# Optimization experiments

Measured on AMD Instinct MI355X. Metric: run time of the kernel, lower is better.

## Reference

```python
import jax, jax.numpy as jnp
import numpy as np

IN_F = 512
OUT_F = 512
ALPHA = 0.2  # LeakyReLU negative slope
# dropout p=0.1 is a no-op at inference (training=False), so omitted


def setup_inputs() -> dict:
    key = jax.random.key(0)
    k1, k2, k3 = jax.random.split(key, 3)
    B, N = 16, 1024
    x = jax.random.normal(k1, (B, N, IN_F), dtype=jnp.float32)
    # xavier_uniform with gain=1.414
    limW = 1.414 * np.sqrt(6.0 / (IN_F + OUT_F))
    W = jax.random.uniform(k2, (IN_F, OUT_F), minval=-limW, maxval=limW, dtype=jnp.float32)
    lima = 1.414 * np.sqrt(6.0 / (2 * OUT_F + 1))
    a = jax.random.uniform(k3, (2 * OUT_F, 1), minval=-lima, maxval=lima, dtype=jnp.float32)
    beta = jnp.ones((1,), dtype=jnp.float32)
    return {"x": x, "W": W, "a": a, "beta": beta}


def reference(x, W, a, beta):
    # h: [B, N, F]
    h = jnp.matmul(x, W)
    # Split attention vector: e_ij = leakyrelu(h_i . a1 + h_j . a2)
    a1 = a[:OUT_F, 0]   # [F]
    a2 = a[OUT_F:, 0]   # [F]
    s1 = jnp.einsum('bnf,f->bn', h, a1)  # [B, N]
    s2 = jnp.einsum('bnf,f->bn', h, a2)  # [B, N]
    e = s1[:, :, None] + s2[:, None, :]  # [B, N, N]
    e = jnp.where(e > 0, e, ALPHA * e)   # LeakyReLU
    attention = jax.nn.softmax(e, axis=2)
    h_prime = jnp.einsum('bnm,bmf->bnf', attention, h)
    out = jax.nn.elu(h_prime + beta * h)
    return out
```

## Files before the change

### kernel.cpp

```cpp
#include <hip/hip_runtime.h>

using u16 = unsigned short;
using u32 = unsigned int;

#define ALPHA 0.2f
#define LOG2E 1.4426950408889634f

typedef __bf16 bf16x8 __attribute__((ext_vector_type(8)));
typedef float f32x4 __attribute__((ext_vector_type(4)));
typedef float f32x16 __attribute__((ext_vector_type(16)));

__device__ __forceinline__ u16 f2bf(float f) {
  u32 u = __builtin_bit_cast(u32, f);
  u += 0x7FFFu + ((u >> 16) & 1u);
  return (u16)(u >> 16);
}
__device__ __forceinline__ float bf2f(u16 h) {
  u32 u = ((u32)h) << 16;
  return __builtin_bit_cast(float, u);
}
__device__ __forceinline__ void gload_lds16(const void* g, void* l) {
  __builtin_amdgcn_global_load_lds((__attribute__((address_space(1))) void*)g,
                                   (__attribute__((address_space(3))) void*)l,
                                   16, 0, 0);
}

__global__ __launch_bounds__(256) void k_cast_wT(const float* __restrict__ W, u16* __restrict__ wbt) {
  int idx = blockIdx.x * 256 + threadIdx.x;
  int k = idx >> 9, n = idx & 511;
  wbt[n * 512 + k] = f2bf(W[idx]);
}

__global__ __launch_bounds__(256, 2) void k_gemm1(const float* __restrict__ x, const u16* __restrict__ wbt,
                                                  const float* __restrict__ a,
                                                  u16* __restrict__ hbf, u16* __restrict__ hbt,
                                                  float* __restrict__ s1p, float* __restrict__ s2p) {
  __shared__ __attribute__((aligned(16))) char lds[73728];
  __shared__ __attribute__((aligned(16))) float a_l[256];

  const int t = threadIdx.x;
  const int lane = t & 63;
  const int w = t >> 6;
  const int l31 = lane & 31, lhi = lane >> 5;
  const int rb = w >> 1, cg = w & 1;
  const int tile_m = blockIdx.x >> 2;
  const int cb = blockIdx.x & 3;
  const int row0 = tile_m * 128;
  const int col0 = cb * 128;

  a_l[t] = (t < 128) ? a[col0 + t] : a[512 + col0 + (t - 128)];

  f32x16 acc[2][2];
#pragma unroll
  for (int i = 0; i < 2; ++i)
#pragma unroll
    for (int j = 0; j < 2; ++j)
#pragma unroll
      for (int r = 0; r < 16; ++r) acc[i][j][r] = 0.f;

#define STAGE_G1(kt, Ab, Bb)                                                              \
  {                                                                                       \
    const int k0_ = (kt) * 32;                                                            \
    _Pragma("unroll")                                                                     \
    for (int i = 0; i < 4; ++i) {                                                         \
      int G = i * 256 + t;                                                                \
      int row = G >> 3, ks = G & 7;                                                       \
      gload_lds16(x + (size_t)(row0 + row) * 512 + k0_ + ((ks ^ (row & 7)) * 4),          \
                  (Ab) + (size_t)(i * 256 + w * 64) * 16);                                \
    }                                                                                     \
    _Pragma("unroll")                                                                     \
    for (int i = 0; i < 2; ++i) {                                                         \
      int G = i * 256 + t;                                                                \
      int col = G >> 2, ks = G & 3;                                                       \
      gload_lds16(wbt + (size_t)(col0 + col) * 512 + k0_ + ((ks ^ ((col >> 1) & 3)) * 8), \
                  (Bb) + (size_t)(i * 256 + w * 64) * 16);                                \
    }                                                                                     \
  }

#define COMPUTE_G1(Ab, Bb)                                                                         \
  {                                                                                                \
    _Pragma("unroll")                                                                              \
    for (int ks = 0; ks < 2; ++ks) {                                                               \
      bf16x8 af[2];                                                                                \
      _Pragma("unroll")                                                                            \
      for (int sub = 0; sub < 2; ++sub) {                                                          \
        const int arow = rb * 64 + sub * 32 + l31;                                                 \
        const int kg = ks * 4 + lhi * 2;                                                           \
        f32x4 fa0 = *reinterpret_cast<const f32x4*>((Ab) + (size_t)(arow * 8 + (kg ^ (arow & 7))) * 16); \
        f32x4 fa1 = *reinterpret_cast<const f32x4*>((Ab) + (size_t)(arow * 8 + ((kg + 1) ^ (arow & 7))) * 16); \
        _Pragma("unroll")                                                                          \
        for (int j = 0; j < 4; ++j) {                                                              \
          af[sub][j] = (__bf16)fa0[j];                                                             \
          af[sub][j + 4] = (__bf16)fa1[j];                                                         \
        }                                                                                          \
      }                                                                                            \
      bf16x8 bfr[2];                                                                               \
      _Pragma("unroll")                                                                            \
      for (int bt = 0; bt < 2; ++bt) {                                                             \
        const int bcol = cg * 64 + bt * 32 + l31;                                                  \
        const int kslot = (ks * 2 + lhi) ^ ((bcol >> 1) & 3);                                      \
        bfr[bt] = *reinterpret_cast<const bf16x8*>((Bb) + (size_t)(bcol * 4 + kslot) * 16);        \
      }                                                                                            \
      _Pragma("unroll")                                                                            \
      for (int sub = 0; sub < 2; ++sub)                                                            \
        _Pragma("unroll")                                                                          \
        for (int bt = 0; bt < 2; ++bt)                                                             \
          acc[sub][bt] = __builtin_amdgcn_mfma_f32_32x32x16_bf16(af[sub], bfr[bt], acc[sub][bt], 0, 0, 0); \
    }                                                                                              \
  }

  char* Ac = lds;             char* Bc = lds + 49152;
  char* An = lds + 16384;     char* Bn = lds + 57344;
  char* As = lds + 32768;     char* Bs = lds + 65536;

  STAGE_G1(0, Ac, Bc);
  STAGE_G1(1, An, Bn);
  __builtin_amdgcn_sched_barrier(0);
  asm volatile("s_waitcnt vmcnt(6) lgkmcnt(0)" ::: "memory");
  __builtin_amdgcn_s_barrier();
  __builtin_amdgcn_sched_barrier(0);

#pragma unroll 1
  for (int kt = 0; kt < 14; ++kt) {
    STAGE_G1(kt + 2, As, Bs);
    COMPUTE_G1(Ac, Bc);
    __builtin_amdgcn_sched_barrier(0);
    asm volatile("s_waitcnt vmcnt(6)" ::: "memory");
    __builtin_amdgcn_s_barrier();
    __builtin_amdgcn_sched_barrier(0);
    char* ta = Ac; Ac = An; An = As; As = ta;
    char* tb = Bc; Bc = Bn; Bn = Bs; Bs = tb;
  }
  COMPUTE_G1(Ac, Bc);
  __builtin_amdgcn_sched_barrier(0);
  asm volatile("s_waitcnt vmcnt(0)" ::: "memory");
  __builtin_amdgcn_s_barrier();
  __builtin_amdgcn_sched_barrier(0);
  COMPUTE_G1(An, Bn);
#undef STAGE_G1
#undef COMPUTE_G1

  __syncthreads();

  u16* lT = (u16*)lds;
#pragma unroll
  for (int sub = 0; sub < 2; ++sub)
#pragma unroll
    for (int bt = 0; bt < 2; ++bt) {
      const int col = cg * 64 + bt * 32 + l31;
#pragma unroll
      for (int r = 0; r < 16; ++r) {
        int row = rb * 64 + sub * 32 + (r & 3) + 8 * (r >> 2) + 4 * lhi;
        lT[row * 136 + col] = f2bf(acc[sub][bt][r]);
      }
    }
  __syncthreads();

#pragma unroll
  for (int i = 0; i < 8; ++i) {
    int G = i * 256 + t;
    int row = G >> 4, g = G & 15;
    uint4 v = *reinterpret_cast<const uint4*>(&lT[row * 136 + g * 8]);
    *reinterpret_cast<uint4*>(&hbf[(size_t)(row0 + row) * 512 + col0 + g * 8]) = v;
  }
  const int bb = row0 >> 10;
  const int nb = row0 & 1023;
#pragma unroll
  for (int i = 0; i < 8; ++i) {
    int G = i * 256 + t;
    int col = G & 127, rg = G >> 7;
    u32 wd[4];
#pragma unroll
    for (int jj = 0; jj < 4; ++jj) {
      u16 lo = lT[(rg * 8 + 2 * jj) * 136 + col];
      u16 hi = lT[(rg * 8 + 2 * jj + 1) * 136 + col];
      wd[jj] = (u32)lo | ((u32)hi << 16);
    }
    uint4 o = {wd[0], wd[1], wd[2], wd[3]};
    *reinterpret_cast<uint4*>(&hbt[(size_t)(bb * 512 + col0 + col) * 1024 + nb + rg * 8]) = o;
  }
  {
    const int r2 = t >> 1, half = t & 1;
    float d1 = 0.f, d2 = 0.f;
#pragma unroll
    for (int i = 0; i < 8; ++i) {
      uint4 v = *reinterpret_cast<const uint4*>(&lT[r2 * 136 + half * 64 + i * 8]);
      u32 wds[4] = {v.x, v.y, v.z, v.w};
#pragma unroll
      for (int j = 0; j < 8; ++j) {
        float h = bf2f((u16)(wds[j >> 1] >> ((j & 1) * 16)));
        d1 += h * a_l[half * 64 + i * 8 + j];
        d2 += h * a_l[128 + half * 64 + i * 8 + j];
      }
    }
    d1 += __shfl_xor(d1, 1);
    d2 += __shfl_xor(d2, 1);
    if (half == 0) {
      s1p[cb * 16384 + row0 + r2] = d1;
      s2p[cb * 16384 + row0 + r2] = d2;
    }
  }
}

__global__ __launch_bounds__(256) void k_reduce(const float* __restrict__ s1p, const float* __restrict__ s2p,
                                                float* __restrict__ s1L, float* __restrict__ s2L) {
  int id = blockIdx.x * 256 + threadIdx.x;
  float d1 = s1p[id] + s1p[16384 + id] + s1p[32768 + id] + s1p[49152 + id];
  float d2 = s2p[id] + s2p[16384 + id] + s2p[32768 + id] + s2p[49152 + id];
  s1L[id] = d1 * LOG2E;
  s2L[id] = d2 * LOG2E;
}

__global__ __launch_bounds__(256) void k_denom(const float* __restrict__ s1Lg, const float* __restrict__ s2Lg,
                                               float* __restrict__ invg) {
  const int lane = threadIdx.x & 63;
  const int w = threadIdx.x >> 6;
  const int row = blockIdx.x * 4 + w;
  const int b = row >> 10;
  const float s1v = s1Lg[row];
  const float* s2p = s2Lg + ((size_t)b << 10);
  float sum = 0.f;
#pragma unroll
  for (int i = 0; i < 16; ++i) {
    float e = s1v + s2p[i * 64 + lane];
    sum += exp2f(fmaxf(e, ALPHA * e));
  }
#pragma unroll
  for (int off = 32; off > 0; off >>= 1) sum += __shfl_xor(sum, off);
  if (lane == 0) invg[row] = 1.0f / sum;
}

__global__ __launch_bounds__(256, 2) void k_attn(const u16* __restrict__ hbt, const u16* __restrict__ hbf,
                                                 const float* __restrict__ s1Lg, const float* __restrict__ s2Lg,
                                                 const float* __restrict__ invg, const float* __restrict__ betag,
                                                 float* __restrict__ out) {
  __shared__ __attribute__((aligned(16))) u16 bbuf[3][8192];
  __shared__ __attribute__((aligned(16))) float e1_l[1024];
  __shared__ __attribute__((aligned(16))) float e2_l[1024];
  const int t = threadIdx.x;
  const int lane = t & 63;
  const int w = t >> 6;
  const int l31 = lane & 31, lhi = lane >> 5;

  const int B = blockIdx.x;
  const int b = (B & 7) * 2 + ((B >> 3) & 1);
  const int j = B >> 4;
  const int n0 = (j >> 2) * 128;
  const int c0 = (j & 3) * 128;

  const u16* hb = hbt + (size_t)b * 512 * 1024;

  for (int i = t; i < 1024; i += 256) {
    float v = s2Lg[b * 1024 + i];
    e1_l[i] = exp2f(v);
    e2_l[i] = exp2f(ALPHA * v);
  }
  const int myrow = n0 + w * 32 + l31;
  const float s1v = s1Lg[b * 1024 + myrow];
  const float c1 = exp2f(s1v), c2 = exp2f(ALPHA * s1v);

#define STAGE_ATTN(mt, dst)                                                        \
  {                                                                                \
    _Pragma("unroll")                                                              \
    for (int i = 0; i < 4; ++i) {                                                  \
      int G = i * 256 + t;                                                         \
      int c = G >> 3, g = G & 7;                                                   \
      gload_lds16(hb + (size_t)(c0 + c) * 1024 + (mt) * 64 + ((g ^ (c & 7)) * 8),  \
                  (char*)(dst) + (size_t)(i * 256 + w * 64) * 16);                 \
    }                                                                              \
  }

#define COMPUTE_ATTN(mt, src)                                                                 \
  {                                                                                           \
    _Pragma("unroll")                                                                         \
    for (int step = 0; step < 4; ++step) {                                                    \
      const int mo = (mt) * 64 + step * 16 + lhi * 8;                                         \
      f32x4 ea = *reinterpret_cast<const f32x4*>(&e1_l[mo]);                                  \
      f32x4 eb = *reinterpret_cast<const f32x4*>(&e1_l[mo + 4]);                              \
      f32x4 fa = *reinterpret_cast<const f32x4*>(&e2_l[mo]);                                  \
      f32x4 fb = *reinterpret_cast<const f32x4*>(&e2_l[mo + 4]);                              \
      bf16x8 af;                                                                              \
      _Pragma("unroll")                                                                       \
      for (int q = 0; q < 4; ++q) {                                                           \
        af[q] = (__bf16)fmaxf(c1 * ea[q], c2 * fa[q]);                                        \
        af[q + 4] = (__bf16)fmaxf(c1 * eb[q], c2 * fb[q]);                                    \
      }                                                                                       \
      const int gm = step * 2 + lhi;                                                          \
      _Pragma("unroll")                                                                       \
      for (int ct = 0; ct < 4; ++ct) {                                                        \
        const int c = ct * 32 + l31;                                                          \
        bf16x8 bv = *reinterpret_cast<const bf16x8*>(&(src)[c * 64 + ((gm ^ (c & 7)) * 8)]);  \
        acc[ct] = __builtin_amdgcn_mfma_f32_32x32x16_bf16(af, bv, acc[ct], 0, 0, 0);          \
      }                                                                                       \
    }                                                                                         \
  }

  f32x16 acc[4];
#pragma unroll
  for (int ct = 0; ct < 4; ++ct)
#pragma unroll
    for (int r = 0; r < 16; ++r) acc[ct][r] = 0.f;

  u16* bcur = bbuf[0];
  u16* bnxt = bbuf[1];
  u16* bstg = bbuf[2];

  STAGE_ATTN(0, bcur);
  STAGE_ATTN(1, bnxt);
  __builtin_amdgcn_sched_barrier(0);
  asm volatile("s_waitcnt vmcnt(4) lgkmcnt(0)" ::: "memory");
  __builtin_amdgcn_s_barrier();
  __builtin_amdgcn_sched_barrier(0);

#pragma unroll 1
  for (int mt = 0; mt < 14; ++mt) {
    STAGE_ATTN(mt + 2, bstg);
    COMPUTE_ATTN(mt, bcur);
    __builtin_amdgcn_sched_barrier(0);
    asm volatile("s_waitcnt vmcnt(4)" ::: "memory");
    __builtin_amdgcn_s_barrier();
    __builtin_amdgcn_sched_barrier(0);
    u16* tmp = bcur; bcur = bnxt; bnxt = bstg; bstg = tmp;
  }
  COMPUTE_ATTN(14, bcur);
  __builtin_amdgcn_sched_barrier(0);
  asm volatile("s_waitcnt vmcnt(0)" ::: "memory");
  __builtin_amdgcn_s_barrier();
  __builtin_amdgcn_sched_barrier(0);
  COMPUTE_ATTN(15, bnxt);
#undef STAGE_ATTN
#undef COMPUTE_ATTN

  const float beta = betag[0];
  const float* invb = invg + b * 1024;
  const u16* hf = hbf + (size_t)b * 1024 * 512;
#pragma unroll
  for (int ct = 0; ct < 4; ++ct) {
    const int colv = c0 + ct * 32 + l31;
#pragma unroll
    for (int rg = 0; rg < 4; ++rg) {
      const int rowb = n0 + w * 32 + rg * 8 + lhi * 4;
      f32x4 iv = *reinterpret_cast<const f32x4*>(&invb[rowb]);
#pragma unroll
      for (int q = 0; q < 4; ++q) {
        float hv = bf2f(hf[(size_t)(rowb + q) * 512 + colv]);
        float xv = acc[ct][rg * 4 + q] * iv[q] + beta * hv;
        out[((size_t)b * 1024 + rowb + q) * 512 + colv] = xv > 0.f ? xv : __expf(xv) - 1.0f;
      }
    }
  }
}

extern "C" void kernel_launch(void* const* d_in, const int* in_sizes, int n_in,
                              void* d_out, int out_size, void* d_ws, size_t ws_size,
                              hipStream_t stream) {
  const float* x = (const float*)d_in[0];
  const float* W = (const float*)d_in[1];
  const float* a = (const float*)d_in[2];
  const float* beta = (const float*)d_in[3];
  float* out = (float*)d_out;

  char* ws = (char*)d_ws;
  u16* hbf = (u16*)ws;
  u16* hbt = (u16*)(ws + (16u << 20));
  u16* wbt = (u16*)(ws + (32u << 20));
  float* s1p = (float*)(ws + (32u << 20) + (512u << 10));
  float* s2p = (float*)(ws + (32u << 20) + (768u << 10));
  float* s1L = (float*)(ws + (33u << 20));
  float* s2L = (float*)(ws + (33u << 20) + (64u << 10));
  float* inv = (float*)(ws + (33u << 20) + (128u << 10));

  k_cast_wT<<<1024, 256, 0, stream>>>(W, wbt);
  k_gemm1<<<512, 256, 0, stream>>>(x, wbt, a, hbf, hbt, s1p, s2p);
  k_reduce<<<64, 256, 0, stream>>>(s1p, s2p, s1L, s2L);
  k_denom<<<4096, 256, 0, stream>>>(s1L, s2L, inv);
  k_attn<<<512, 256, 0, stream>>>(hbt, hbf, s1L, s2L, inv, beta, out);
}
```

Measured before the change: 74.59 us.

## Fuse softmax denominator into attention kernel and pre-swizzle H into MFMA fragment layout

Removes the separate k_denom kernel by summing the unnormalised attention weights in registers inside k_attn and reducing them per row. gemm1 now writes the transposed H in a fragment-ready tiled layout, so k_attn loads B operands straight from global memory into registers with one-step prefetch, replacing the LDS triple-buffered staging and its barriers. It also remaps gemm1 block indices so neighbouring blocks share column tiles. This drops a kernel launch and LDS traffic, but leaves the global loads with less latency hiding. The row sums now come from bf16-bound fp32 values rather than the separate exact pass.

```diff
diff --git a/kernel.cpp b/kernel.cpp
--- a/kernel.cpp
+++ b/kernel.cpp
@@ -31,9 +31,10 @@
   wbt[n * 512 + k] = f2bf(W[idx]);
 }
 
+
 __global__ __launch_bounds__(256, 2) void k_gemm1(const float* __restrict__ x, const u16* __restrict__ wbt,
                                                   const float* __restrict__ a,
-                                                  u16* __restrict__ hbf, u16* __restrict__ hbt,
+                                                  u16* __restrict__ hbf, u16* __restrict__ hbt2,
                                                   float* __restrict__ s1p, float* __restrict__ s2p) {
   __shared__ __attribute__((aligned(16))) char lds[73728];
   __shared__ __attribute__((aligned(16))) float a_l[256];
@@ -43,8 +44,9 @@
   const int w = t >> 6;
   const int l31 = lane & 31, lhi = lane >> 5;
   const int rb = w >> 1, cg = w & 1;
-  const int tile_m = blockIdx.x >> 2;
-  const int cb = blockIdx.x & 3;
+  const int g = blockIdx.x;
+  const int cb = (g >> 3) & 3;
+  const int tile_m = (g & 7) | ((g >> 5) << 3);
   const int row0 = tile_m * 128;
   const int col0 = cb * 128;
 
@@ -89,9 +91,9 @@
         f32x4 fa0 = *reinterpret_cast<const f32x4*>((Ab) + (size_t)(arow * 8 + (kg ^ (arow & 7))) * 16); \
         f32x4 fa1 = *reinterpret_cast<const f32x4*>((Ab) + (size_t)(arow * 8 + ((kg + 1) ^ (arow & 7))) * 16); \
         _Pragma("unroll")                                                                          \
-        for (int j = 0; j < 4; ++j) {                                                              \
-          af[sub][j] = (__bf16)fa0[j];                                                             \
-          af[sub][j + 4] = (__bf16)fa1[j];                                                         \
+        for (int jj = 0; jj < 4; ++jj) {                                                           \
+          af[sub][jj] = (__bf16)fa0[jj];                                                           \
+          af[sub][jj + 4] = (__bf16)fa1[jj];                                                       \
         }                                                                                          \
       }                                                                                            \
       bf16x8 bfr[2];                                                                               \
@@ -159,12 +161,13 @@
 #pragma unroll
   for (int i = 0; i < 8; ++i) {
     int G = i * 256 + t;
-    int row = G >> 4, g = G & 15;
-    uint4 v = *reinterpret_cast<const uint4*>(&lT[row * 136 + g * 8]);
-    *reinterpret_cast<uint4*>(&hbf[(size_t)(row0 + row) * 512 + col0 + g * 8]) = v;
+    int row = G >> 4, gg = G & 15;
+    uint4 v = *reinterpret_cast<const uint4*>(&lT[row * 136 + gg * 8]);
+    *reinterpret_cast<uint4*>(&hbf[(size_t)(row0 + row) * 512 + col0 + gg * 8]) = v;
   }
   const int bb = row0 >> 10;
   const int nb = row0 & 1023;
+  u16* hb2 = hbt2 + (size_t)bb * 524288;
 #pragma unroll
   for (int i = 0; i < 8; ++i) {
     int G = i * 256 + t;
@@ -177,7 +180,10 @@
       wd[jj] = (u32)lo | ((u32)hi << 16);
     }
     uint4 o = {wd[0], wd[1], wd[2], wd[3]};
-    *reinterpret_cast<uint4*>(&hbt[(size_t)(bb * 512 + col0 + col) * 1024 + nb + rg * 8]) = o;
+    const int m0 = nb + rg * 8;
+    const int f = col0 + col;
+    size_t idx = (size_t)(m0 >> 4) * 8192 + (size_t)(f >> 5) * 512 + (size_t)((m0 >> 3) & 1) * 256 + (size_t)(f & 31) * 8;
+    *reinterpret_cast<uint4*>(&hb2[idx]) = o;
   }
   {
     const int r2 = t >> 1, half = t & 1;
@@ -187,10 +193,10 @@
       uint4 v = *reinterpret_cast<const uint4*>(&lT[r2 * 136 + half * 64 + i * 8]);
       u32 wds[4] = {v.x, v.y, v.z, v.w};
 #pragma unroll
-      for (int j = 0; j < 8; ++j) {
-        float h = bf2f((u16)(wds[j >> 1] >> ((j & 1) * 16)));
-        d1 += h * a_l[half * 64 + i * 8 + j];
-        d2 += h * a_l[128 + half * 64 + i * 8 + j];
+      for (int jj = 0; jj < 8; ++jj) {
+        float h = bf2f((u16)(wds[jj >> 1] >> ((jj & 1) * 16)));
+        d1 += h * a_l[half * 64 + i * 8 + jj];
+        d2 += h * a_l[128 + half * 64 + i * 8 + jj];
       }
     }
     d1 += __shfl_xor(d1, 1);
@@ -211,32 +217,12 @@
   s2L[id] = d2 * LOG2E;
 }
 
-__global__ __launch_bounds__(256) void k_denom(const float* __restrict__ s1Lg, const float* __restrict__ s2Lg,
-                                               float* __restrict__ invg) {
-  const int lane = threadIdx.x & 63;
-  const int w = threadIdx.x >> 6;
-  const int row = blockIdx.x * 4 + w;
-  const int b = row >> 10;
-  const float s1v = s1Lg[row];
-  const float* s2p = s2Lg + ((size_t)b << 10);
-  float sum = 0.f;
-#pragma unroll
-  for (int i = 0; i < 16; ++i) {
-    float e = s1v + s2p[i * 64 + lane];
-    sum += exp2f(fmaxf(e, ALPHA * e));
-  }
-#pragma unroll
-  for (int off = 32; off > 0; off >>= 1) sum += __shfl_xor(sum, off);
-  if (lane == 0) invg[row] = 1.0f / sum;
-}
-
-__global__ __launch_bounds__(256, 2) void k_attn(const u16* __restrict__ hbt, const u16* __restrict__ hbf,
+__global__ __launch_bounds__(256, 2) void k_attn(const u16* __restrict__ hbt2, const u16* __restrict__ hbf,
                                                  const float* __restrict__ s1Lg, const float* __restrict__ s2Lg,
-                                                 const float* __restrict__ invg, const float* __restrict__ betag,
-                                                 float* __restrict__ out) {
-  __shared__ __attribute__((aligned(16))) u16 bbuf[3][8192];
+                                                 const float* __restrict__ betag, float* __restrict__ out) {
   __shared__ __attribute__((aligned(16))) float e1_l[1024];
   __shared__ __attribute__((aligned(16))) float e2_l[1024];
+  __shared__ __attribute__((aligned(16))) float inv_l[128];
   const int t = threadIdx.x;
   const int lane = t & 63;
   const int w = t >> 6;
@@ -248,99 +234,81 @@
   const int n0 = (j >> 2) * 128;
   const int c0 = (j & 3) * 128;
 
-  const u16* hb = hbt + (size_t)b * 512 * 1024;
+  const u16* hb2 = hbt2 + (size_t)b * 524288;
 
   for (int i = t; i < 1024; i += 256) {
     float v = s2Lg[b * 1024 + i];
     e1_l[i] = exp2f(v);
     e2_l[i] = exp2f(ALPHA * v);
   }
+
   const int myrow = n0 + w * 32 + l31;
   const float s1v = s1Lg[b * 1024 + myrow];
   const float c1 = exp2f(s1v), c2 = exp2f(ALPHA * s1v);
 
-#define STAGE_ATTN(mt, dst)                                                        \
-  {                                                                                \
-    _Pragma("unroll")                                                              \
-    for (int i = 0; i < 4; ++i) {                                                  \
-      int G = i * 256 + t;                                                         \
-      int c = G >> 3, g = G & 7;                                                   \
-      gload_lds16(hb + (size_t)(c0 + c) * 1024 + (mt) * 64 + ((g ^ (c & 7)) * 8),  \
-                  (char*)(dst) + (size_t)(i * 256 + w * 64) * 16);                 \
-    }                                                                              \
-  }
-
-#define COMPUTE_ATTN(mt, src)                                                                 \
-  {                                                                                           \
-    _Pragma("unroll")                                                                         \
-    for (int step = 0; step < 4; ++step) {                                                    \
-      const int mo = (mt) * 64 + step * 16 + lhi * 8;                                         \
-      f32x4 ea = *reinterpret_cast<const f32x4*>(&e1_l[mo]);                                  \
-      f32x4 eb = *reinterpret_cast<const f32x4*>(&e1_l[mo + 4]);                              \
-      f32x4 fa = *reinterpret_cast<const f32x4*>(&e2_l[mo]);                                  \
-      f32x4 fb = *reinterpret_cast<const f32x4*>(&e2_l[mo + 4]);                              \
-      bf16x8 af;                                                                              \
-      _Pragma("unroll")                                                                       \
-      for (int q = 0; q < 4; ++q) {                                                           \
-        af[q] = (__bf16)fmaxf(c1 * ea[q], c2 * fa[q]);                                        \
-        af[q + 4] = (__bf16)fmaxf(c1 * eb[q], c2 * fb[q]);                                    \
-      }                                                                                       \
-      const int gm = step * 2 + lhi;                                                          \
-      _Pragma("unroll")                                                                       \
-      for (int ct = 0; ct < 4; ++ct) {                                                        \
-        const int c = ct * 32 + l31;                                                          \
-        bf16x8 bv = *reinterpret_cast<const bf16x8*>(&(src)[c * 64 + ((gm ^ (c & 7)) * 8)]);  \
-        acc[ct] = __builtin_amdgcn_mfma_f32_32x32x16_bf16(af, bv, acc[ct], 0, 0, 0);          \
-      }                                                                                       \
-    }                                                                                         \
-  }
-
   f32x16 acc[4];
 #pragma unroll
   for (int ct = 0; ct < 4; ++ct)
 #pragma unroll
     for (int r = 0; r < 16; ++r) acc[ct][r] = 0.f;
-
-  u16* bcur = bbuf[0];
-  u16* bnxt = bbuf[1];
-  u16* bstg = bbuf[2];
-
-  STAGE_ATTN(0, bcur);
-  STAGE_ATTN(1, bnxt);
-  __builtin_amdgcn_sched_barrier(0);
-  asm volatile("s_waitcnt vmcnt(4) lgkmcnt(0)" ::: "memory");
-  __builtin_amdgcn_s_barrier();
-  __builtin_amdgcn_sched_barrier(0);
-
-#pragma unroll 1
-  for (int mt = 0; mt < 14; ++mt) {
-    STAGE_ATTN(mt + 2, bstg);
-    COMPUTE_ATTN(mt, bcur);
-    __builtin_amdgcn_sched_barrier(0);
-    asm volatile("s_waitcnt vmcnt(4)" ::: "memory");
-    __builtin_amdgcn_s_barrier();
-    __builtin_amdgcn_sched_barrier(0);
-    u16* tmp = bcur; bcur = bnxt; bnxt = bstg; bstg = tmp;
-  }
-  COMPUTE_ATTN(14, bcur);
-  __builtin_amdgcn_sched_barrier(0);
-  asm volatile("s_waitcnt vmcnt(0)" ::: "memory");
-  __builtin_amdgcn_s_barrier();
-  __builtin_amdgcn_sched_barrier(0);
-  COMPUTE_ATTN(15, bnxt);
-#undef STAGE_ATTN
-#undef COMPUTE_ATTN
+  float psum = 0.f;
+
+  __syncthreads();
+
+  const u16* bp = hb2 + (size_t)(c0 >> 5) * 512 + (size_t)(lhi * 32 + l31) * 8;
+
+#define STEP_ATTN(s, buf)                                                      \
+  {                                                                            \
+    const int mo = (s) * 16 + lhi * 8;                                         \
+    f32x4 ea = *reinterpret_cast<const f32x4*>(&e1_l[mo]);                     \
+    f32x4 eb = *reinterpret_cast<const f32x4*>(&e1_l[mo + 4]);                 \
+    f32x4 fa = *reinterpret_cast<const f32x4*>(&e2_l[mo]);                     \
+    f32x4 fb = *reinterpret_cast<const f32x4*>(&e2_l[mo + 4]);                 \
+    bf16x8 af;                                                                 \
+    _Pragma("unroll")                                                          \
+    for (int q = 0; q < 4; ++q) {                                              \
+      float p0 = fmaxf(c1 * ea[q], c2 * fa[q]);                                \
+      float p1 = fmaxf(c1 * eb[q], c2 * fb[q]);                                \
+      psum += p0 + p1;                                                         \
+      af[q] = (__bf16)p0;                                                      \
+      af[q + 4] = (__bf16)p1;                                                  \
+    }                                                                          \
+    _Pragma("unroll")                                                          \
+    for (int ct = 0; ct < 4; ++ct)                                             \
+      acc[ct] = __builtin_amdgcn_mfma_f32_32x32x16_bf16(af, (buf)[ct], acc[ct], 0, 0, 0); \
+  }
+
+  bf16x8 bv[4];
+#pragma unroll
+  for (int ct = 0; ct < 4; ++ct) bv[ct] = *reinterpret_cast<const bf16x8*>(bp + ct * 512);
+
+#pragma unroll 4
+  for (int s = 0; s < 63; ++s) {
+    bf16x8 nv[4];
+    const u16* np = bp + (size_t)(s + 1) * 8192;
+#pragma unroll
+    for (int ct = 0; ct < 4; ++ct) nv[ct] = *reinterpret_cast<const bf16x8*>(np + ct * 512);
+    STEP_ATTN(s, bv);
+#pragma unroll
+    for (int ct = 0; ct < 4; ++ct) bv[ct] = nv[ct];
+  }
+  STEP_ATTN(63, bv);
+#undef STEP_ATTN
+
+  psum += __shfl_xor(psum, 32);
+  if (lhi == 0) inv_l[w * 32 + l31] = 1.0f / psum;
+  __syncthreads();
 
   const float beta = betag[0];
-  const float* invb = invg + b * 1024;
   const u16* hf = hbf + (size_t)b * 1024 * 512;
 #pragma unroll
   for (int ct = 0; ct < 4; ++ct) {
     const int colv = c0 + ct * 32 + l31;
 #pragma unroll
     for (int rg = 0; rg < 4; ++rg) {
-      const int rowb = n0 + w * 32 + rg * 8 + lhi * 4;
-      f32x4 iv = *reinterpret_cast<const f32x4*>(&invb[rowb]);
+      const int rl = rg * 8 + lhi * 4;
+      const int rowb = n0 + w * 32 + rl;
+      f32x4 iv = *reinterpret_cast<const f32x4*>(&inv_l[w * 32 + rl]);
 #pragma unroll
       for (int q = 0; q < 4; ++q) {
         float hv = bf2f(hf[(size_t)(rowb + q) * 512 + colv]);
@@ -362,17 +330,15 @@
 
   char* ws = (char*)d_ws;
   u16* hbf = (u16*)ws;
-  u16* hbt = (u16*)(ws + (16u << 20));
+  u16* hbt2 = (u16*)(ws + (16u << 20));
   u16* wbt = (u16*)(ws + (32u << 20));
   float* s1p = (float*)(ws + (32u << 20) + (512u << 10));
   float* s2p = (float*)(ws + (32u << 20) + (768u << 10));
   float* s1L = (float*)(ws + (33u << 20));
   float* s2L = (float*)(ws + (33u << 20) + (64u << 10));
-  float* inv = (float*)(ws + (33u << 20) + (128u << 10));
 
   k_cast_wT<<<1024, 256, 0, stream>>>(W, wbt);
-  k_gemm1<<<512, 256, 0, stream>>>(x, wbt, a, hbf, hbt, s1p, s2p);
+  k_gemm1<<<512, 256, 0, stream>>>(x, wbt, a, hbf, hbt2, s1p, s2p);
   k_reduce<<<64, 256, 0, stream>>>(s1p, s2p, s1L, s2L);
-  k_denom<<<4096, 256, 0, stream>>>(s1L, s2L, inv);
-  k_attn<<<512, 256, 0, stream>>>(hbt, hbf, s1L, s2L, inv, beta, out);
-}
+  k_attn<<<512, 256, 0, stream>>>(hbt2, hbf, s1L, s2L, beta, out);
+}
```

After: 71.51 us. 1.04x faster.
